# Performance work log

Measured on AMD Instinct MI355X. Metric: run time of the kernel, lower is better.

The kernel has to match this reference:

```python
import jax, jax.numpy as jnp
import numpy as np

B = 8192
NUM_SAMPLES = 128
RESAMPLE_PADDING = 0.01
F32_EPS = float(np.finfo(np.float32).eps)


def lift_gaussian_diag(d, t_mean, t_var, r_var):
    # d: [B,3]; t_mean/t_var/r_var: [B,S]
    mean = d[..., None, :] * t_mean[..., None]                      # [B,S,3]
    d_mag_sq = jnp.clip(jnp.sum(d ** 2, axis=-1, keepdims=True), 1e-10)
    d_outer_diag = d ** 2
    null_outer_diag = 1.0 - d_outer_diag / d_mag_sq
    cov_diag = (t_var[..., None] * d_outer_diag[..., None, :]
                + r_var[..., None] * null_outer_diag[..., None, :])  # [B,S,3]
    return mean, cov_diag


def conical_frustum_to_gaussian(d, t0, t1, base_radius):
    # stable=True branch of the original code
    mu = (t0 + t1) / 2
    hw = (t1 - t0) / 2
    t_mean = mu + 2 * mu * hw ** 2 / (3 * mu ** 2 + hw ** 2)
    t_var = hw ** 2 / 3 - 4 / 15 * (hw ** 4 * (12 * mu ** 2 - hw ** 2)
                                    / (3 * mu ** 2 + hw ** 2) ** 2)
    r_var = base_radius ** 2 * (mu ** 2 / 4 + 5 / 12 * hw ** 2
                                - 4 / 15 * hw ** 4 / (3 * mu ** 2 + hw ** 2))
    return lift_gaussian_diag(d, t_mean, t_var, r_var)


def cast_rays(t_vals, origins, directions, radii):
    # ray_shape == 'cone', diag == True
    means, covs = conical_frustum_to_gaussian(
        directions, t_vals[..., :-1], t_vals[..., 1:], radii)
    return means + origins[..., None, :], covs


def sorted_piecewise_constant_pdf(bins, weights, num_samples):
    # randomized=False branch; faithful O(n*m) mask-based interval search
    eps = 1e-5
    weight_sum = jnp.sum(weights, axis=-1, keepdims=True)
    padding = jnp.clip(eps - weight_sum, 0)
    weights = weights + padding / weights.shape[-1]
    weight_sum = weight_sum + padding
    pdf = weights / weight_sum
    cdf = jnp.minimum(jnp.cumsum(pdf[..., :-1], axis=-1), 1.0)
    z = jnp.zeros(cdf.shape[:-1] + (1,), cdf.dtype)
    o = jnp.ones(cdf.shape[:-1] + (1,), cdf.dtype)
    cdf = jnp.concatenate([z, cdf, o], axis=-1)                      # [B, nb+1]
    u = jnp.linspace(0.0, 1.0 - F32_EPS, num_samples, dtype=cdf.dtype)
    u = jnp.broadcast_to(u, cdf.shape[:-1] + (num_samples,))         # [B, S]
    mask = u[..., None, :] >= cdf[..., :, None]                      # [B, nb+1, S]

    def find_interval(x):
        x0 = jnp.max(jnp.where(mask, x[..., None], x[..., :1, None]), axis=-2)
        x1 = jnp.min(jnp.where(~mask, x[..., None], x[..., -1:, None]), axis=-2)
        return x0, x1

    bins_g0, bins_g1 = find_interval(bins)
    cdf_g0, cdf_g1 = find_interval(cdf)
    t = jnp.clip(jnp.nan_to_num((u - cdf_g0) / (cdf_g1 - cdf_g0)), 0, 1)
    return bins_g0 + t * (bins_g1 - bins_g0)


def setup_inputs() -> dict:
    key = jax.random.key(0)
    k0, k1, k2, k3 = jax.random.split(key, 4)
    origins = jax.random.normal(k0, (B, 3), dtype=jnp.float32)
    directions = jax.random.normal(k1, (B, 3), dtype=jnp.float32)
    directions = directions / jnp.linalg.norm(directions, axis=-1, keepdims=True)
    radii = 0.001 + 0.01 * jax.random.uniform(k2, (B, 1), dtype=jnp.float32)
    near = 2.0 * jnp.ones((B, 1), dtype=jnp.float32)
    far = 6.0 * jnp.ones((B, 1), dtype=jnp.float32)
    weights = jax.random.uniform(k3, (B, NUM_SAMPLES), dtype=jnp.float32)
    return {"origins": origins, "directions": directions, "radii": radii,
            "near": near, "far": far, "weights": weights}


def reference(origins, directions, radii, near, far, weights):
    # coarse stratified sampling (randomized=False, lindisp=False)
    t = jnp.linspace(0.0, 1.0, NUM_SAMPLES + 1, dtype=jnp.float32)
    t_coarse = near * (1.0 - t) + far * t                            # [B, S+1]
    means_c, covs_c = cast_rays(t_coarse, origins, directions, radii)
    # resample_along_rays: blur weights then inverse-CDF sample
    wpad = jnp.concatenate([weights[..., :1], weights, weights[..., -1:]], axis=-1)
    wmax = jnp.maximum(wpad[..., :-1], wpad[..., 1:])
    wblur = 0.5 * (wmax[..., :-1] + wmax[..., 1:]) + RESAMPLE_PADDING
    t_fine = sorted_piecewise_constant_pdf(t_coarse, wblur, t_coarse.shape[-1])
    means_f, covs_f = cast_rays(t_fine, origins, directions, radii)
    return (t_coarse, means_c, covs_c, t_fine, means_f, covs_f)
```

## Files before the change

kernel.cpp:

```cpp
#include <hip/hip_runtime.h>


constexpr int B_RAYS = 8192;
constexpr int S      = 128;
constexpr int SP1    = 129;
constexpr float F32_EPS = 1.1920928955078125e-07f;

constexpr long long O_TC = 0;
constexpr long long O_MC = O_TC + (long long)B_RAYS * SP1;
constexpr long long O_CC = O_MC + (long long)B_RAYS * S * 3;
constexpr long long O_TF = O_CC + (long long)B_RAYS * S * 3;
constexpr long long O_MF = O_TF + (long long)B_RAYS * SP1;
constexpr long long O_CF = O_MF + (long long)B_RAYS * S * 3;

__device__ __forceinline__ void frustum(float t0, float t1, float rad2,
                                        float& tm, float& tv, float& rv)
{
    float mu  = 0.5f * (t0 + t1);
    float hw  = 0.5f * (t1 - t0);
    float mu2 = mu * mu, hw2 = hw * hw, hw4 = hw2 * hw2;
    float den = 3.0f * mu2 + hw2;
    float rden = 1.0f / den;
    tm = mu + (2.0f * mu * hw2) * rden;
    tv = hw2 * (1.0f / 3.0f)
       - (4.0f / 15.0f) * (hw4 * (12.0f * mu2 - hw2)) * (rden * rden);
    rv = rad2 * (0.25f * mu2 + (5.0f / 12.0f) * hw2 - (4.0f / 15.0f) * hw4 * rden);
}

__device__ __forceinline__ float sel3(int c, float x, float y, float z)
{
    return (c == 0) ? x : ((c == 1) ? y : z);
}

__global__ __launch_bounds__(256) void mipnerf_kernel(
    const float* __restrict__ origins,
    const float* __restrict__ directions,
    const float* __restrict__ radii,
    const float* __restrict__ nearp,
    const float* __restrict__ farp,
    const float* __restrict__ weights,
    float* __restrict__ out)
{
    const int tid = threadIdx.x;
    const int w   = tid >> 6;
    const int l   = tid & 63;
    const int b   = (blockIdx.x << 2) + w;

    __shared__ float s_tm[4][128];
    __shared__ float s_tv[4][128];
    __shared__ float s_rv[4][128];
    __shared__ float s_cdf[4][132];
    __shared__ float s_tf[4][132];

    const float ox = origins[3*b+0], oy = origins[3*b+1], oz = origins[3*b+2];
    const float dx = directions[3*b+0], dy = directions[3*b+1], dz = directions[3*b+2];
    const float rad  = radii[b];
    const float rad2 = rad * rad;
    const float nv = nearp[b], fv = farp[b];
    const float dmag2 = fmaxf(dx*dx + dy*dy + dz*dz, 1e-10f);
    const float axx = dx*dx, ayy = dy*dy, azz = dz*dz;
    const float nxx = 1.0f - axx/dmag2, nyy = 1.0f - ayy/dmag2, nzz = 1.0f - azz/dmag2;

    auto bin = [&](int k) {
        float t = (float)k * (1.0f / 128.0f);
        return nv * (1.0f - t) + fv * t;
    };

    auto write_cast = [&](float* __restrict__ om, float* __restrict__ oc) {
        #pragma unroll
        for (int j = 0; j < 3; ++j) {
            int f0 = 2 * (l + 64*j);
            int ia = f0 / 3,      ca = f0 - 3*ia;
            int ib2 = (f0+1) / 3, cb = (f0+1) - 3*ib2;
            float tma = s_tm[w][ia], tmb = s_tm[w][ib2];
            float2 mv;
            mv.x = sel3(ca, dx, dy, dz) * tma + sel3(ca, ox, oy, oz);
            mv.y = sel3(cb, dx, dy, dz) * tmb + sel3(cb, ox, oy, oz);
            *reinterpret_cast<float2*>(om + f0) = mv;
            float2 cv;
            cv.x = s_tv[w][ia] * sel3(ca, axx, ayy, azz)
                 + s_rv[w][ia] * sel3(ca, nxx, nyy, nzz);
            cv.y = s_tv[w][ib2] * sel3(cb, axx, ayy, azz)
                 + s_rv[w][ib2] * sel3(cb, nxx, nyy, nzz);
            *reinterpret_cast<float2*>(oc + f0) = cv;
        }
    };

    for (int s = l; s < SP1; s += 64)
        out[O_TC + (long long)b * SP1 + s] = bin(s);

    #pragma unroll
    for (int j = 0; j < 2; ++j) {
        int i = l + 64*j;
        float tm, tv, rv;
        frustum(bin(i), bin(i+1), rad2, tm, tv, rv);
        s_tm[w][i] = tm; s_tv[w][i] = tv; s_rv[w][i] = rv;
    }
    __builtin_amdgcn_wave_barrier();

    write_cast(out + O_MC + (long long)b * 384, out + O_CC + (long long)b * 384);
    __builtin_amdgcn_wave_barrier();

    float2 wv = *reinterpret_cast<const float2*>(weights + (long long)b * S + 2*l);
    float wprev = __shfl_up(wv.y, 1);   if (l == 0)  wprev = wv.x;
    float wnext = __shfl_down(wv.x, 1); if (l == 63) wnext = wv.y;
    float m0 = fmaxf(wprev, wv.x), m1 = fmaxf(wv.x, wv.y), m2 = fmaxf(wv.y, wnext);
    float wb0 = 0.5f * (m0 + m1) + 0.01f;
    float wb1 = 0.5f * (m1 + m2) + 0.01f;

    float ps   = wb0 + wb1;
    float incl = ps;
    #pragma unroll
    for (int off = 1; off < 64; off <<= 1) {
        float y = __shfl_up(incl, off);
        if (l >= off) incl += y;
    }
    float total = __shfl(incl, 63);
    float pad   = fmaxf(1e-5f - total, 0.0f);
    float wstot = total + pad;
    float inv   = 1.0f / wstot;
    float padk  = pad * (1.0f / 128.0f);
    float excl  = incl - ps;

    float c1 = fminf((excl + wb0 + (float)(2*l + 1) * padk) * inv, 1.0f);
    float c2 = fminf((incl        + (float)(2*l + 2) * padk) * inv, 1.0f);
    s_cdf[w][2*l + 1] = c1;
    s_cdf[w][2*l + 2] = (l == 63) ? 1.0f : c2;
    if (l == 0) s_cdf[w][0] = 0.0f;
    __builtin_amdgcn_wave_barrier();

    const float ustep = (1.0f - F32_EPS) * (1.0f / 128.0f);
    for (int s = l; s < SP1; s += 64) {
        float u = (float)s * ustep;
        int lo = 0, hi = 128;
        #pragma unroll
        for (int it = 0; it < 7; ++it) {
            int mid = (lo + hi) >> 1;
            if (s_cdf[w][mid] <= u) lo = mid; else hi = mid;
        }
        float c0  = s_cdf[w][lo], cg1 = s_cdf[w][lo + 1];
        float tt  = (u - c0) / (cg1 - c0);
        if (!(tt == tt)) tt = 0.0f;
        tt = fminf(fmaxf(tt, 0.0f), 1.0f);
        float b0  = bin(lo);
        float tf  = b0 + tt * (bin(lo + 1) - b0);
        s_tf[w][s] = tf;
        out[O_TF + (long long)b * SP1 + s] = tf;
    }
    __builtin_amdgcn_wave_barrier();

    #pragma unroll
    for (int j = 0; j < 2; ++j) {
        int i = l + 64*j;
        float tm, tv, rv;
        frustum(s_tf[w][i], s_tf[w][i+1], rad2, tm, tv, rv);
        s_tm[w][i] = tm; s_tv[w][i] = tv; s_rv[w][i] = rv;
    }
    __builtin_amdgcn_wave_barrier();

    write_cast(out + O_MF + (long long)b * 384, out + O_CF + (long long)b * 384);
}

extern "C" void kernel_launch(void* const* d_in, const int* in_sizes, int n_in,
                              void* d_out, int out_size, void* d_ws, size_t ws_size,
                              hipStream_t stream)
{
    const float* origins    = (const float*)d_in[0];
    const float* directions = (const float*)d_in[1];
    const float* radii      = (const float*)d_in[2];
    const float* nearp      = (const float*)d_in[3];
    const float* farp       = (const float*)d_in[4];
    const float* weights    = (const float*)d_in[5];
    float* out = (float*)d_out;

    mipnerf_kernel<<<B_RAYS / 4, 256, 0, stream>>>(
        origins, directions, radii, nearp, farp, weights, out);
}
```

Baseline: 19.64 us.

## Compute frustum per float4 output chunk, drop LDS staging, interleave binary searches

The separate frustum pass that staged tm/tv/rv in shared memory is removed. Each lane now computes the two frustums needed for a 4-float output chunk on the fly and writes float4 stores for means and covariances. The three binary searches per lane are interleaved so their LDS loads overlap, and the weights load is moved to the start of the kernel. In exchange, some frustum math is recomputed and half the lanes sit idle in the second chunk pass.

Result: slower. 21.17 us (+7.8%).

```diff
diff --git a/kernel.cpp b/kernel.cpp
--- a/kernel.cpp
+++ b/kernel.cpp
@@ -13,18 +13,20 @@
 constexpr long long O_MF = O_TF + (long long)B_RAYS * SP1;
 constexpr long long O_CF = O_MF + (long long)B_RAYS * S * 3;
 
-__device__ __forceinline__ void frustum(float t0, float t1, float rad2,
-                                        float& tm, float& tv, float& rv)
+struct Frust { float tm, tv, rv; };
+
+__device__ __forceinline__ Frust frustum(float t0, float t1, float rad2)
 {
+    Frust f;
     float mu  = 0.5f * (t0 + t1);
     float hw  = 0.5f * (t1 - t0);
     float mu2 = mu * mu, hw2 = hw * hw, hw4 = hw2 * hw2;
-    float den = 3.0f * mu2 + hw2;
-    float rden = 1.0f / den;
-    tm = mu + (2.0f * mu * hw2) * rden;
-    tv = hw2 * (1.0f / 3.0f)
-       - (4.0f / 15.0f) * (hw4 * (12.0f * mu2 - hw2)) * (rden * rden);
-    rv = rad2 * (0.25f * mu2 + (5.0f / 12.0f) * hw2 - (4.0f / 15.0f) * hw4 * rden);
+    float den = 3.0f * mu2 + hw2, rden = 1.0f / den;
+    f.tm = mu + (2.0f * mu * hw2) * rden;
+    f.tv = hw2 * (1.0f / 3.0f)
+         - (4.0f / 15.0f) * (hw4 * (12.0f * mu2 - hw2)) * (rden * rden);
+    f.rv = rad2 * (0.25f * mu2 + (5.0f / 12.0f) * hw2 - (4.0f / 15.0f) * hw4 * rden);
+    return f;
 }
 
 __device__ __forceinline__ float sel3(int c, float x, float y, float z)
@@ -46,17 +48,16 @@
     const int l   = tid & 63;
     const int b   = (blockIdx.x << 2) + w;
 
-    __shared__ float s_tm[4][128];
-    __shared__ float s_tv[4][128];
-    __shared__ float s_rv[4][128];
     __shared__ float s_cdf[4][132];
     __shared__ float s_tf[4][132];
 
+    const float2 wv = *reinterpret_cast<const float2*>(weights + (long long)b * S + 2*l);
     const float ox = origins[3*b+0], oy = origins[3*b+1], oz = origins[3*b+2];
     const float dx = directions[3*b+0], dy = directions[3*b+1], dz = directions[3*b+2];
-    const float rad  = radii[b];
-    const float rad2 = rad * rad;
+    const float rad = radii[b];
     const float nv = nearp[b], fv = farp[b];
+
+    const float rad2  = rad * rad;
     const float dmag2 = fmaxf(dx*dx + dy*dy + dz*dz, 1e-10f);
     const float axx = dx*dx, ayy = dy*dy, azz = dz*dz;
     const float nxx = 1.0f - axx/dmag2, nyy = 1.0f - ayy/dmag2, nzz = 1.0f - azz/dmag2;
@@ -66,42 +67,47 @@
         return nv * (1.0f - t) + fv * t;
     };
 
-    auto write_cast = [&](float* __restrict__ om, float* __restrict__ oc) {
+    auto emit4 = [&](float ta, float tb, float tc, int m,
+                     float* __restrict__ om, float* __restrict__ oc) {
+        Frust A = frustum(ta, tb, rad2);
+        Frust B = frustum(tb, tc, rad2);
+        int r = m - 3 * (m / 3);
+        float4 mv, cv;
         #pragma unroll
-        for (int j = 0; j < 3; ++j) {
-            int f0 = 2 * (l + 64*j);
-            int ia = f0 / 3,      ca = f0 - 3*ia;
-            int ib2 = (f0+1) / 3, cb = (f0+1) - 3*ib2;
-            float tma = s_tm[w][ia], tmb = s_tm[w][ib2];
-            float2 mv;
-            mv.x = sel3(ca, dx, dy, dz) * tma + sel3(ca, ox, oy, oz);
-            mv.y = sel3(cb, dx, dy, dz) * tmb + sel3(cb, ox, oy, oz);
-            *reinterpret_cast<float2*>(om + f0) = mv;
-            float2 cv;
-            cv.x = s_tv[w][ia] * sel3(ca, axx, ayy, azz)
-                 + s_rv[w][ia] * sel3(ca, nxx, nyy, nzz);
-            cv.y = s_tv[w][ib2] * sel3(cb, axx, ayy, azz)
-                 + s_rv[w][ib2] * sel3(cb, nxx, nyy, nzz);
-            *reinterpret_cast<float2*>(oc + f0) = cv;
+        for (int e = 0; e < 4; ++e) {
+            int  rc   = r + e;
+            bool useB = rc >= 3;
+            int  c    = useB ? rc - 3 : rc;
+            float tm = useB ? B.tm : A.tm;
+            float tv = useB ? B.tv : A.tv;
+            float rv = useB ? B.rv : A.rv;
+            (&mv.x)[e] = sel3(c, dx, dy, dz) * tm + sel3(c, ox, oy, oz);
+            (&cv.x)[e] = tv * sel3(c, axx, ayy, azz) + rv * sel3(c, nxx, nyy, nzz);
         }
+        *reinterpret_cast<float4*>(om + 4*m) = mv;
+        *reinterpret_cast<float4*>(oc + 4*m) = cv;
     };
 
-    for (int s = l; s < SP1; s += 64)
-        out[O_TC + (long long)b * SP1 + s] = bin(s);
+    {
+        float* ot = out + O_TC + (long long)b * SP1;
+        ot[l]      = bin(l);
+        ot[l + 64] = bin(l + 64);
+        if (l == 0) ot[128] = bin(128);
+    }
 
-    #pragma unroll
-    for (int j = 0; j < 2; ++j) {
-        int i = l + 64*j;
-        float tm, tv, rv;
-        frustum(bin(i), bin(i+1), rad2, tm, tv, rv);
-        s_tm[w][i] = tm; s_tv[w][i] = tv; s_rv[w][i] = rv;
+    {
+        float* om = out + O_MC + (long long)b * 384;
+        float* oc = out + O_CC + (long long)b * 384;
+        int m  = l;
+        int k0 = m + m / 3;
+        emit4(bin(k0), bin(k0 + 1), bin(k0 + 2), m, om, oc);
+        if (l < 32) {
+            m  = l + 64;
+            k0 = m + m / 3;
+            emit4(bin(k0), bin(k0 + 1), bin(k0 + 2), m, om, oc);
+        }
     }
-    __builtin_amdgcn_wave_barrier();
 
-    write_cast(out + O_MC + (long long)b * 384, out + O_CC + (long long)b * 384);
-    __builtin_amdgcn_wave_barrier();
-
-    float2 wv = *reinterpret_cast<const float2*>(weights + (long long)b * S + 2*l);
     float wprev = __shfl_up(wv.y, 1);   if (l == 0)  wprev = wv.x;
     float wnext = __shfl_down(wv.x, 1); if (l == 63) wnext = wv.y;
     float m0 = fmaxf(wprev, wv.x), m1 = fmaxf(wv.x, wv.y), m2 = fmaxf(wv.y, wnext);
@@ -130,35 +136,49 @@
     __builtin_amdgcn_wave_barrier();
 
     const float ustep = (1.0f - F32_EPS) * (1.0f / 128.0f);
-    for (int s = l; s < SP1; s += 64) {
-        float u = (float)s * ustep;
-        int lo = 0, hi = 128;
-        #pragma unroll
-        for (int it = 0; it < 7; ++it) {
-            int mid = (lo + hi) >> 1;
-            if (s_cdf[w][mid] <= u) lo = mid; else hi = mid;
-        }
+    const float u0 = (float)l * ustep;
+    const float u1 = (float)(l + 64) * ustep;
+    const float u2 = 128.0f * ustep;
+    int lo0 = 0, hi0 = 128, lo1 = 0, hi1 = 128, lo2 = 0, hi2 = 128;
+    #pragma unroll
+    for (int it = 0; it < 7; ++it) {
+        int q0 = (lo0 + hi0) >> 1, q1 = (lo1 + hi1) >> 1, q2 = (lo2 + hi2) >> 1;
+        float a0 = s_cdf[w][q0], a1 = s_cdf[w][q1], a2 = s_cdf[w][q2];
+        if (a0 <= u0) lo0 = q0; else hi0 = q0;
+        if (a1 <= u1) lo1 = q1; else hi1 = q1;
+        if (a2 <= u2) lo2 = q2; else hi2 = q2;
+    }
+    auto interp = [&](float u, int lo) {
         float c0  = s_cdf[w][lo], cg1 = s_cdf[w][lo + 1];
         float tt  = (u - c0) / (cg1 - c0);
         if (!(tt == tt)) tt = 0.0f;
         tt = fminf(fmaxf(tt, 0.0f), 1.0f);
-        float b0  = bin(lo);
-        float tf  = b0 + tt * (bin(lo + 1) - b0);
-        s_tf[w][s] = tf;
-        out[O_TF + (long long)b * SP1 + s] = tf;
+        float b0 = bin(lo);
+        return b0 + tt * (bin(lo + 1) - b0);
+    };
+    float tf0 = interp(u0, lo0);
+    float tf1 = interp(u1, lo1);
+    float tf2 = interp(u2, lo2);
+    {
+        float* ot = out + O_TF + (long long)b * SP1;
+        s_tf[w][l]      = tf0;  ot[l]      = tf0;
+        s_tf[w][l + 64] = tf1;  ot[l + 64] = tf1;
+        if (l == 0) { s_tf[w][128] = tf2; ot[128] = tf2; }
     }
     __builtin_amdgcn_wave_barrier();
 
-    #pragma unroll
-    for (int j = 0; j < 2; ++j) {
-        int i = l + 64*j;
-        float tm, tv, rv;
-        frustum(s_tf[w][i], s_tf[w][i+1], rad2, tm, tv, rv);
-        s_tm[w][i] = tm; s_tv[w][i] = tv; s_rv[w][i] = rv;
+    {
+        float* om = out + O_MF + (long long)b * 384;
+        float* oc = out + O_CF + (long long)b * 384;
+        int m  = l;
+        int k0 = m + m / 3;
+        emit4(s_tf[w][k0], s_tf[w][k0 + 1], s_tf[w][k0 + 2], m, om, oc);
+        if (l < 32) {
+            m  = l + 64;
+            k0 = m + m / 3;
+            emit4(s_tf[w][k0], s_tf[w][k0 + 1], s_tf[w][k0 + 2], m, om, oc);
+        }
     }
-    __builtin_amdgcn_wave_barrier();
-
-    write_cast(out + O_MF + (long long)b * 384, out + O_CF + (long long)b * 384);
 }
 
 extern "C" void kernel_launch(void* const* d_in, const int* in_sizes, int n_in,
```
